# Optimization experiments

Measured on AMD Instinct MI355X. Metric: run time of the kernel, lower is better.

## Reference

```python
import jax, jax.numpy as jnp
import numpy as np
from jax import lax

TAU = 2.0      # tau_s
V_TH = 0.5     # spike threshold
ALPHA = 2.0    # ATan surrogate width

@jax.custom_vjp
def spike_fn(v):
    return (v >= V_TH).astype(v.dtype)

def _spike_fwd(v):
    return spike_fn(v), v

def _spike_bwd(v, g):
    sg = (ALPHA / 2.0) / (1.0 + (jnp.pi / 2.0 * ALPHA * (v - V_TH)) ** 2)
    return (g * sg,)

spike_fn.defvjp(_spike_fwd, _spike_bwd)

T, B, S = 4, 128, 64
D_STATE = D_TAU = D_EVENT = 3136
FUSION, HIDDEN, LAST = 512, 512, 18

def setup_inputs() -> dict:
    key = jax.random.key(0)
    ks = jax.random.split(key, 10)
    def w(k, i, o):
        return jax.random.normal(k, (i, o), jnp.float32) / np.sqrt(i)
    return {
        'state_embedding': jax.random.normal(ks[0], (T, B, D_STATE), jnp.float32),
        'tau_embedding': jax.random.normal(ks[1], (T, B * S, D_TAU), jnp.float32),
        'eventspikes_embedding': jax.random.normal(ks[2], (T, B, D_EVENT), jnp.float32),
        'W_prox': w(ks[3], D_STATE, FUSION),
        'W_dist': w(ks[4], D_TAU, FUSION),
        'W_trunk': w(ks[5], D_EVENT, FUSION),
        'W1': w(ks[6], FUSION, HIDDEN),
        'b1': jnp.zeros((HIDDEN,), jnp.float32),
        'W2': w(ks[7], HIDDEN, LAST),
        'b2': jnp.zeros((LAST,), jnp.float32),
    }

def reference(state_embedding, tau_embedding, eventspikes_embedding,
              W_prox, W_dist, W_trunk, W1, b1, W2, b2):
    t_win, bsz, _ = state_embedding.shape
    ssz = tau_embedding.shape[1] // bsz
    fsz = W_prox.shape[1]
    hsz = W1.shape[1]

    def step(carry, xs):
        p, d, t, soma, lif_mem = carry
        se, te, ee = xs
        prox = (se @ W_prox)[:, None, :]              # [B,1,F]
        dist = (te @ W_dist).reshape(bsz, ssz, fsz)   # [B,S,F]
        trunk = (ee @ W_trunk)[:, None, :]            # [B,1,F]
        # multi-compartment LIF integration
        p = p + (prox - p) / TAU
        d = d + (dist - d) / TAU
        t = t + (trunk - t) / TAU
        soma = soma + (p * d + t - soma) / TAU        # [B,S,F]
        s = spike_fn(soma)
        soma = soma * (1.0 - s)
        emb = s.reshape(bsz * ssz, fsz)
        # _last: Linear -> LIF -> Linear
        h = emb @ W1 + b1
        lif_mem = lif_mem + (h - lif_mem) / TAU
        hs = spike_fn(lif_mem)
        lif_mem = lif_mem * (1.0 - hs)
        out = hs @ W2 + b2                            # [B*S, LAST]
        return (p, d, t, soma, lif_mem), out

    z = jnp.zeros
    init = (z((bsz, 1, fsz)), z((bsz, ssz, fsz)), z((bsz, 1, fsz)),
            z((bsz, ssz, fsz)), z((bsz * ssz, hsz)))
    _, outs = lax.scan(step, init, (state_embedding, tau_embedding, eventspikes_embedding))
    q = outs.mean(0)                                  # average over time window
    return q.reshape(bsz, ssz, -1).transpose(0, 2, 1)  # [B, LAST, S]
```

## Files before the change

### kernel.cpp

```cpp
#include <hip/hip_runtime.h>
#include <stdint.h>

typedef __attribute__((ext_vector_type(4))) float f32x4;

#define T_WIN 4
#define BSZ   128
#define SSZ   64
#define DDIM  3136
#define FDIM  512
#define HDIM  512
#define LDIM  18
#define ROWS  8192
#define KB    16

struct GArgs { const void* A; const float* B; float* C; int M; };

template<int AMODE, int FIRST>
__global__ __launch_bounds__(128, 2) void sgemm_pass(GArgs g0, GArgs g1, GArgs g2,
                                                     int N, int K, int ks, int ke) {
  GArgs g = g0;
  if (blockIdx.z == 1) g = g1;
  else if (blockIdx.z == 2) g = g2;
  const int m0 = blockIdx.x * 128;
  if (m0 >= g.M) return;
  const int n0 = blockIdx.y * 128;

  __shared__ float sA[KB][256];
  __shared__ float sB[KB][132];

  const int tid = threadIdx.x;
  const int tx = tid & 15;
  const int ty = tid >> 4;

  const int am = tid;
  const int br = tid >> 3;
  const int bc = (tid & 7) * 16;

  const float*   Af = (const float*)g.A;
  const uint8_t* A8 = (const uint8_t*)g.A;

  float acc[16][8];
#pragma unroll
  for (int i = 0; i < 16; i++)
#pragma unroll
    for (int j = 0; j < 8; j++) acc[i][j] = 0.f;

  for (int k0 = ks; k0 < ke; k0 += KB) {
    f32x4 av[4];
    if (AMODE == 0) {
      const float* ap = Af + (size_t)(m0 + am) * K + k0;
#pragma unroll
      for (int c = 0; c < 4; c++) av[c] = *(const f32x4*)(ap + 4 * c);
    } else {
      uint4 wrd = *(const uint4*)(A8 + (size_t)(m0 + am) * K + k0);
      uint32_t u[4] = {wrd.x, wrd.y, wrd.z, wrd.w};
#pragma unroll
      for (int c = 0; c < 4; c++) {
        av[c][0] = (float)(u[c] & 255u);
        av[c][1] = (float)((u[c] >> 8) & 255u);
        av[c][2] = (float)((u[c] >> 16) & 255u);
        av[c][3] = (float)((u[c] >> 24) & 255u);
      }
    }
    f32x4 bv[4];
    const float* bp = g.B + (size_t)(k0 + br) * N + n0 + bc;
#pragma unroll
    for (int c = 0; c < 4; c++) bv[c] = *(const f32x4*)(bp + 4 * c);

    __syncthreads();
#pragma unroll
    for (int c = 0; c < 4; c++)
#pragma unroll
      for (int j = 0; j < 4; j++)
        sA[4 * c + j][am] = av[c][j];
#pragma unroll
    for (int c = 0; c < 4; c++)
      *(f32x4*)&sB[br][bc + 4 * c] = bv[c];
    __syncthreads();

#pragma unroll 2
    for (int k = 0; k < KB; k++) {
      f32x4 a0 = *(const f32x4*)&sA[k][ty * 16];
      f32x4 a1 = *(const f32x4*)&sA[k][ty * 16 + 4];
      f32x4 a2 = *(const f32x4*)&sA[k][ty * 16 + 8];
      f32x4 a3 = *(const f32x4*)&sA[k][ty * 16 + 12];
      f32x4 b0 = *(const f32x4*)&sB[k][tx * 4];
      f32x4 b1 = *(const f32x4*)&sB[k][64 + tx * 4];
      float a[16] = {a0[0], a0[1], a0[2], a0[3], a1[0], a1[1], a1[2], a1[3],
                     a2[0], a2[1], a2[2], a2[3], a3[0], a3[1], a3[2], a3[3]};
      float b[8]  = {b0[0], b0[1], b0[2], b0[3], b1[0], b1[1], b1[2], b1[3]};
#pragma unroll
      for (int i = 0; i < 16; i++)
#pragma unroll
        for (int j = 0; j < 8; j++)
          acc[i][j] = __fmaf_rn(a[i], b[j], acc[i][j]);
    }
  }

#pragma unroll
  for (int i = 0; i < 16; i++) {
    float* cp = g.C + (size_t)(m0 + ty * 16 + i) * N + n0;
    f32x4 v0 = {acc[i][0], acc[i][1], acc[i][2], acc[i][3]};
    f32x4 v1 = {acc[i][4], acc[i][5], acc[i][6], acc[i][7]};
    if (FIRST) {
      *(f32x4*)(cp + tx * 4) = v0;
      *(f32x4*)(cp + 64 + tx * 4) = v1;
    } else {
      f32x4 o0 = *(const f32x4*)(cp + tx * 4);
      f32x4 o1 = *(const f32x4*)(cp + 64 + tx * 4);
#pragma unroll
      for (int c = 0; c < 4; c++) { v0[c] = __fadd_rn(o0[c], v0[c]); v1[c] = __fadd_rn(o1[c], v1[c]); }
      *(f32x4*)(cp + tx * 4) = v0;
      *(f32x4*)(cp + 64 + tx * 4) = v1;
    }
  }
}

__global__ __launch_bounds__(256) void filter_pt_kernel(const float* __restrict__ prox,
                                                        const float* __restrict__ trunk,
                                                        float* __restrict__ P,
                                                        float* __restrict__ Tf) {
  int idx = blockIdx.x * 256 + threadIdx.x;
  int b = idx >> 7;
  int fc = (idx & 127) << 2;
  f32x4 p = {0.f, 0.f, 0.f, 0.f}, t = {0.f, 0.f, 0.f, 0.f};
  for (int tt = 0; tt < T_WIN; tt++) {
    size_t o = (size_t)(tt * BSZ + b) * FDIM + fc;
    f32x4 x = *(const f32x4*)&prox[o];
    f32x4 y = *(const f32x4*)&trunk[o];
#pragma unroll
    for (int c = 0; c < 4; c++) {
      p[c] = __fadd_rn(p[c], __fmul_rn(__fsub_rn(x[c], p[c]), 0.5f));
      t[c] = __fadd_rn(t[c], __fmul_rn(__fsub_rn(y[c], t[c]), 0.5f));
    }
    *(f32x4*)&P[o] = p;
    *(f32x4*)&Tf[o] = t;
  }
}

__global__ __launch_bounds__(256) void lif_soma_kernel(const float* __restrict__ dist,
                                                       const float* __restrict__ P,
                                                       const float* __restrict__ Tf,
                                                       uint8_t* __restrict__ emb) {
  int idx = blockIdx.x * 256 + threadIdx.x;
  int r = idx >> 7;
  int fc = (idx & 127) << 2;
  int b = r >> 6;
  f32x4 d = {0.f, 0.f, 0.f, 0.f}, soma = {0.f, 0.f, 0.f, 0.f};
#pragma unroll
  for (int t = 0; t < T_WIN; t++) {
    f32x4 x  = *(const f32x4*)&dist[(size_t)(t * ROWS + r) * FDIM + fc];
    f32x4 pv = *(const f32x4*)&P[(size_t)(t * BSZ + b) * FDIM + fc];
    f32x4 tv = *(const f32x4*)&Tf[(size_t)(t * BSZ + b) * FDIM + fc];
    uint32_t bits = 0;
#pragma unroll
    for (int c = 0; c < 4; c++) {
      d[c] = __fadd_rn(d[c], __fmul_rn(__fsub_rn(x[c], d[c]), 0.5f));
      float pd = __fmul_rn(pv[c], d[c]);
      float u  = __fadd_rn(pd, tv[c]);
      float w  = __fsub_rn(u, soma[c]);
      soma[c] = __fadd_rn(soma[c], __fmul_rn(w, 0.5f));
      if (soma[c] >= 0.5f) { bits |= (1u << (8 * c)); soma[c] = 0.f; }
    }
    *(uint32_t*)&emb[(size_t)(t * ROWS + r) * FDIM + fc] = bits;
  }
}

__global__ __launch_bounds__(256) void lif_hidden_kernel(const float* __restrict__ H,
                                                         const float* __restrict__ b1,
                                                         uint8_t* __restrict__ cnt) {
  int idx = blockIdx.x * 256 + threadIdx.x;
  int r = idx >> 7;
  int fc = (idx & 127) << 2;
  f32x4 bb = *(const f32x4*)&b1[fc];
  f32x4 lif = {0.f, 0.f, 0.f, 0.f};
  uint32_t counts = 0;
#pragma unroll
  for (int t = 0; t < T_WIN; t++) {
    f32x4 h = *(const f32x4*)&H[(size_t)(t * ROWS + r) * FDIM + fc];
#pragma unroll
    for (int c = 0; c < 4; c++) {
      float hv = __fadd_rn(h[c], bb[c]);
      lif[c] = __fadd_rn(lif[c], __fmul_rn(__fsub_rn(hv, lif[c]), 0.5f));
      if (lif[c] >= 0.5f) { counts += (1u << (8 * c)); lif[c] = 0.f; }
    }
  }
  *(uint32_t*)&cnt[(size_t)r * FDIM + fc] = counts;
}

__global__ __launch_bounds__(256) void out_kernel(const uint8_t* __restrict__ cnt,
                                                  const float* __restrict__ W2,
                                                  const float* __restrict__ b2,
                                                  float* __restrict__ out) {
  int idx = blockIdx.x * 256 + threadIdx.x;
  int r = idx / LDIM;
  int j = idx - r * LDIM;
  const uint4* crow = (const uint4*)(cnt + (size_t)r * HDIM);
  float acc = 0.f;
  for (int q = 0; q < HDIM / 16; q++) {
    uint4 wrd = crow[q];
    uint32_t u[4] = {wrd.x, wrd.y, wrd.z, wrd.w};
#pragma unroll
    for (int wq = 0; wq < 4; wq++)
#pragma unroll
      for (int s = 0; s < 4; s++) {
        uint32_t c = (u[wq] >> (8 * s)) & 255u;
        if (c) acc = __fmaf_rn((float)c * 0.25f, W2[(16 * q + 4 * wq + s) * LDIM + j], acc);
      }
  }
  int b = r >> 6, s = r & 63;
  out[(size_t)b * (LDIM * SSZ) + j * SSZ + s] = __fadd_rn(acc, b2[j]);
}


extern "C" void kernel_launch(void* const* d_in, const int* in_sizes, int n_in,
                              void* d_out, int out_size, void* d_ws, size_t ws_size,
                              hipStream_t stream) {
  const float* se     = (const float*)d_in[0];
  const float* te     = (const float*)d_in[1];
  const float* ee     = (const float*)d_in[2];
  const float* Wprox  = (const float*)d_in[3];
  const float* Wdist  = (const float*)d_in[4];
  const float* Wtrunk = (const float*)d_in[5];
  const float* W1     = (const float*)d_in[6];
  const float* b1     = (const float*)d_in[7];
  const float* W2     = (const float*)d_in[8];
  const float* b2     = (const float*)d_in[9];

  char* ws = (char*)d_ws;
  float*   dist_all  = (float*)(ws);
  uint8_t* emb8      = (uint8_t*)(ws + 67108864);
  uint8_t* cnt8      = (uint8_t*)(ws + 83886080);
  float*   prox_raw  = (float*)(ws + 88080384);
  float*   trunk_raw = (float*)(ws + 89128960);
  float*   P         = (float*)(ws + 90177536);
  float*   Tf        = (float*)(ws + 91226112);

  static const int KC[10] = {0, 384, 768, 1152, 1536, 1920, 2304, 2688, 2912, 3136};

  GArgs gd{te, Wdist, dist_all, T_WIN * ROWS};
  GArgs gp{se, Wprox, prox_raw, T_WIN * BSZ};
  GArgs gt{ee, Wtrunk, trunk_raw, T_WIN * BSZ};
  {
    dim3 gg(256, 4, 3), bb(128);
    sgemm_pass<0, 1><<<gg, bb, 0, stream>>>(gd, gp, gt, FDIM, DDIM, KC[0], KC[1]);
    for (int p = 1; p < 9; p++)
      sgemm_pass<0, 0><<<gg, bb, 0, stream>>>(gd, gp, gt, FDIM, DDIM, KC[p], KC[p + 1]);
  }

  filter_pt_kernel<<<64, 256, 0, stream>>>(prox_raw, trunk_raw, P, Tf);

  lif_soma_kernel<<<4096, 256, 0, stream>>>(dist_all, P, Tf, emb8);

  GArgs gh{emb8, W1, dist_all, T_WIN * ROWS};
  {
    dim3 gg(256, 4, 1), bb(128);
    sgemm_pass<1, 1><<<gg, bb, 0, stream>>>(gh, gh, gh, HDIM, FDIM, 0, 256);
    sgemm_pass<1, 0><<<gg, bb, 0, stream>>>(gh, gh, gh, HDIM, FDIM, 256, 512);
  }

  lif_hidden_kernel<<<4096, 256, 0, stream>>>(dist_all, b1, cnt8);

  out_kernel<<<576, 256, 0, stream>>>(cnt8, W2, b2, (float*)d_out);
}
```

Before: 2.403 ms.

## Replace sequential split-K passes with one launch writing per-chunk partials

The nine sequential split-K GEMM launches (each reading back and adding the previous partial) become one launch with the K-chunk on grid z. Each chunk writes its own partial buffer, and the downstream LIF kernels sum the 9 (or 2) partials in the same fixed order. The grid is also compacted so the small prox/trunk GEMMs no longer launch mostly-empty blocks, and the inner loop gains register prefetch of the next tile. This removes per-pass launch gaps and read-modify-write traffic, but the partial buffers take about 600 MB of workspace that the LIF kernels must then read back.

Measured after the change: 2.116 ms. 12.0% less time.

```diff
diff --git a/kernel.cpp b/kernel.cpp
--- a/kernel.cpp
+++ b/kernel.cpp
@@ -15,15 +15,28 @@
 
 struct GArgs { const void* A; const float* B; float* C; int M; };
 
-template<int AMODE, int FIRST>
-__global__ __launch_bounds__(128, 2) void sgemm_pass(GArgs g0, GArgs g1, GArgs g2,
-                                                     int N, int K, int ks, int ke) {
+__device__ __forceinline__ void kchunk3136(int z, int& ks, int& ke) {
+  ks = (z <= 7) ? 384 * z : 2912;
+  ke = (z <= 6) ? 384 * (z + 1) : ((z == 7) ? 2912 : 3136);
+}
+
+template<int AMODE, int SMALLS>
+__global__ __launch_bounds__(128, 2) void gemm_chunks(GArgs g0, GArgs g1, GArgs g2,
+                                                      int N, int K, int kcmode) {
+  int xb = blockIdx.x;
   GArgs g = g0;
-  if (blockIdx.z == 1) g = g1;
-  else if (blockIdx.z == 2) g = g2;
-  const int m0 = blockIdx.x * 128;
-  if (m0 >= g.M) return;
+  if (SMALLS && xb >= 256) {
+    int idx = xb - 256;
+    g = (idx >> 2) ? g2 : g1;
+    xb = idx & 3;
+  }
+  int ks, ke;
+  if (kcmode == 0) kchunk3136(blockIdx.z, ks, ke);
+  else { ks = blockIdx.z * 256; ke = ks + 256; }
+
+  const int m0 = xb * 128;
   const int n0 = blockIdx.y * 128;
+  float* C = g.C + (size_t)blockIdx.z * g.M * N;
 
   __shared__ float sA[KB][256];
   __shared__ float sB[KB][132];
@@ -45,8 +58,8 @@
 #pragma unroll
     for (int j = 0; j < 8; j++) acc[i][j] = 0.f;
 
-  for (int k0 = ks; k0 < ke; k0 += KB) {
-    f32x4 av[4];
+  f32x4 av[4], bv[4];
+  auto load_step = [&](int k0) {
     if (AMODE == 0) {
       const float* ap = Af + (size_t)(m0 + am) * K + k0;
 #pragma unroll
@@ -62,11 +75,13 @@
         av[c][3] = (float)((u[c] >> 24) & 255u);
       }
     }
-    f32x4 bv[4];
     const float* bp = g.B + (size_t)(k0 + br) * N + n0 + bc;
 #pragma unroll
     for (int c = 0; c < 4; c++) bv[c] = *(const f32x4*)(bp + 4 * c);
-
+  };
+
+  load_step(ks);
+  for (int k0 = ks; k0 < ke; k0 += KB) {
     __syncthreads();
 #pragma unroll
     for (int c = 0; c < 4; c++)
@@ -78,7 +93,9 @@
       *(f32x4*)&sB[br][bc + 4 * c] = bv[c];
     __syncthreads();
 
-#pragma unroll 2
+    if (k0 + KB < ke) load_step(k0 + KB);
+
+#pragma unroll 4
     for (int k = 0; k < KB; k++) {
       f32x4 a0 = *(const f32x4*)&sA[k][ty * 16];
       f32x4 a1 = *(const f32x4*)&sA[k][ty * 16 + 4];
@@ -99,35 +116,33 @@
 
 #pragma unroll
   for (int i = 0; i < 16; i++) {
-    float* cp = g.C + (size_t)(m0 + ty * 16 + i) * N + n0;
+    float* cp = C + (size_t)(m0 + ty * 16 + i) * N + n0;
     f32x4 v0 = {acc[i][0], acc[i][1], acc[i][2], acc[i][3]};
     f32x4 v1 = {acc[i][4], acc[i][5], acc[i][6], acc[i][7]};
-    if (FIRST) {
-      *(f32x4*)(cp + tx * 4) = v0;
-      *(f32x4*)(cp + 64 + tx * 4) = v1;
-    } else {
-      f32x4 o0 = *(const f32x4*)(cp + tx * 4);
-      f32x4 o1 = *(const f32x4*)(cp + 64 + tx * 4);
-#pragma unroll
-      for (int c = 0; c < 4; c++) { v0[c] = __fadd_rn(o0[c], v0[c]); v1[c] = __fadd_rn(o1[c], v1[c]); }
-      *(f32x4*)(cp + tx * 4) = v0;
-      *(f32x4*)(cp + 64 + tx * 4) = v1;
-    }
-  }
-}
-
-__global__ __launch_bounds__(256) void filter_pt_kernel(const float* __restrict__ prox,
-                                                        const float* __restrict__ trunk,
-                                                        float* __restrict__ P,
-                                                        float* __restrict__ Tf) {
+    *(f32x4*)(cp + tx * 4) = v0;
+    *(f32x4*)(cp + 64 + tx * 4) = v1;
+  }
+}
+
+__global__ __launch_bounds__(256) void filter_pt9(const float* __restrict__ Cp,
+                                                  const float* __restrict__ Ct,
+                                                  float* __restrict__ P,
+                                                  float* __restrict__ Tf) {
+  const size_t CH = (size_t)T_WIN * BSZ * FDIM;
   int idx = blockIdx.x * 256 + threadIdx.x;
   int b = idx >> 7;
   int fc = (idx & 127) << 2;
   f32x4 p = {0.f, 0.f, 0.f, 0.f}, t = {0.f, 0.f, 0.f, 0.f};
   for (int tt = 0; tt < T_WIN; tt++) {
     size_t o = (size_t)(tt * BSZ + b) * FDIM + fc;
-    f32x4 x = *(const f32x4*)&prox[o];
-    f32x4 y = *(const f32x4*)&trunk[o];
+    f32x4 x = *(const f32x4*)&Cp[o];
+    f32x4 y = *(const f32x4*)&Ct[o];
+    for (int q = 1; q < 9; q++) {
+      f32x4 xq = *(const f32x4*)&Cp[o + q * CH];
+      f32x4 yq = *(const f32x4*)&Ct[o + q * CH];
+#pragma unroll
+      for (int c = 0; c < 4; c++) { x[c] = __fadd_rn(x[c], xq[c]); y[c] = __fadd_rn(y[c], yq[c]); }
+    }
 #pragma unroll
     for (int c = 0; c < 4; c++) {
       p[c] = __fadd_rn(p[c], __fmul_rn(__fsub_rn(x[c], p[c]), 0.5f));
@@ -138,10 +153,11 @@
   }
 }
 
-__global__ __launch_bounds__(256) void lif_soma_kernel(const float* __restrict__ dist,
-                                                       const float* __restrict__ P,
-                                                       const float* __restrict__ Tf,
-                                                       uint8_t* __restrict__ emb) {
+__global__ __launch_bounds__(256) void lif_soma9(const float* __restrict__ Cd,
+                                                 const float* __restrict__ P,
+                                                 const float* __restrict__ Tf,
+                                                 uint8_t* __restrict__ emb) {
+  const size_t CH = (size_t)T_WIN * ROWS * FDIM;
   int idx = blockIdx.x * 256 + threadIdx.x;
   int r = idx >> 7;
   int fc = (idx & 127) << 2;
@@ -149,7 +165,14 @@
   f32x4 d = {0.f, 0.f, 0.f, 0.f}, soma = {0.f, 0.f, 0.f, 0.f};
 #pragma unroll
   for (int t = 0; t < T_WIN; t++) {
-    f32x4 x  = *(const f32x4*)&dist[(size_t)(t * ROWS + r) * FDIM + fc];
+    size_t o = (size_t)(t * ROWS + r) * FDIM + fc;
+    f32x4 x = *(const f32x4*)&Cd[o];
+#pragma unroll
+    for (int q = 1; q < 9; q++) {
+      f32x4 xq = *(const f32x4*)&Cd[o + q * CH];
+#pragma unroll
+      for (int c = 0; c < 4; c++) x[c] = __fadd_rn(x[c], xq[c]);
+    }
     f32x4 pv = *(const f32x4*)&P[(size_t)(t * BSZ + b) * FDIM + fc];
     f32x4 tv = *(const f32x4*)&Tf[(size_t)(t * BSZ + b) * FDIM + fc];
     uint32_t bits = 0;
@@ -162,13 +185,14 @@
       soma[c] = __fadd_rn(soma[c], __fmul_rn(w, 0.5f));
       if (soma[c] >= 0.5f) { bits |= (1u << (8 * c)); soma[c] = 0.f; }
     }
-    *(uint32_t*)&emb[(size_t)(t * ROWS + r) * FDIM + fc] = bits;
-  }
-}
-
-__global__ __launch_bounds__(256) void lif_hidden_kernel(const float* __restrict__ H,
-                                                         const float* __restrict__ b1,
-                                                         uint8_t* __restrict__ cnt) {
+    *(uint32_t*)&emb[o] = bits;
+  }
+}
+
+__global__ __launch_bounds__(256) void lif_hidden2(const float* __restrict__ Hc,
+                                                   const float* __restrict__ b1,
+                                                   uint8_t* __restrict__ cnt) {
+  const size_t CH = (size_t)T_WIN * ROWS * FDIM;
   int idx = blockIdx.x * 256 + threadIdx.x;
   int r = idx >> 7;
   int fc = (idx & 127) << 2;
@@ -177,10 +201,12 @@
   uint32_t counts = 0;
 #pragma unroll
   for (int t = 0; t < T_WIN; t++) {
-    f32x4 h = *(const f32x4*)&H[(size_t)(t * ROWS + r) * FDIM + fc];
+    size_t o = (size_t)(t * ROWS + r) * FDIM + fc;
+    f32x4 h0 = *(const f32x4*)&Hc[o];
+    f32x4 h1 = *(const f32x4*)&Hc[o + CH];
 #pragma unroll
     for (int c = 0; c < 4; c++) {
-      float hv = __fadd_rn(h[c], bb[c]);
+      float hv = __fadd_rn(__fadd_rn(h0[c], h1[c]), bb[c]);
       lif[c] = __fadd_rn(lif[c], __fmul_rn(__fsub_rn(hv, lif[c]), 0.5f));
       if (lif[c] >= 0.5f) { counts += (1u << (8 * c)); lif[c] = 0.f; }
     }
@@ -228,38 +254,28 @@
   const float* b2     = (const float*)d_in[9];
 
   char* ws = (char*)d_ws;
-  float*   dist_all  = (float*)(ws);
-  uint8_t* emb8      = (uint8_t*)(ws + 67108864);
-  uint8_t* cnt8      = (uint8_t*)(ws + 83886080);
-  float*   prox_raw  = (float*)(ws + 88080384);
-  float*   trunk_raw = (float*)(ws + 89128960);
-  float*   P         = (float*)(ws + 90177536);
-  float*   Tf        = (float*)(ws + 91226112);
-
-  static const int KC[10] = {0, 384, 768, 1152, 1536, 1920, 2304, 2688, 2912, 3136};
-
-  GArgs gd{te, Wdist, dist_all, T_WIN * ROWS};
-  GArgs gp{se, Wprox, prox_raw, T_WIN * BSZ};
-  GArgs gt{ee, Wtrunk, trunk_raw, T_WIN * BSZ};
-  {
-    dim3 gg(256, 4, 3), bb(128);
-    sgemm_pass<0, 1><<<gg, bb, 0, stream>>>(gd, gp, gt, FDIM, DDIM, KC[0], KC[1]);
-    for (int p = 1; p < 9; p++)
-      sgemm_pass<0, 0><<<gg, bb, 0, stream>>>(gd, gp, gt, FDIM, DDIM, KC[p], KC[p + 1]);
-  }
-
-  filter_pt_kernel<<<64, 256, 0, stream>>>(prox_raw, trunk_raw, P, Tf);
-
-  lif_soma_kernel<<<4096, 256, 0, stream>>>(dist_all, P, Tf, emb8);
-
-  GArgs gh{emb8, W1, dist_all, T_WIN * ROWS};
-  {
-    dim3 gg(256, 4, 1), bb(128);
-    sgemm_pass<1, 1><<<gg, bb, 0, stream>>>(gh, gh, gh, HDIM, FDIM, 0, 256);
-    sgemm_pass<1, 0><<<gg, bb, 0, stream>>>(gh, gh, gh, HDIM, FDIM, 256, 512);
-  }
-
-  lif_hidden_kernel<<<4096, 256, 0, stream>>>(dist_all, b1, cnt8);
+  float*   Cd   = (float*)(ws);
+  float*   Hc   = (float*)(ws);
+  float*   Cp   = (float*)(ws + 603979776);
+  float*   Ct   = (float*)(ws + 613416960);
+  float*   P    = (float*)(ws + 622854144);
+  float*   Tf   = (float*)(ws + 623902720);
+  uint8_t* emb8 = (uint8_t*)(ws + 624951296);
+  uint8_t* cnt8 = (uint8_t*)(ws + 641728512);
+
+  GArgs gd{te, Wdist, Cd, T_WIN * ROWS};
+  GArgs gp{se, Wprox, Cp, T_WIN * BSZ};
+  GArgs gt{ee, Wtrunk, Ct, T_WIN * BSZ};
+  gemm_chunks<0, 1><<<dim3(264, 4, 9), 128, 0, stream>>>(gd, gp, gt, FDIM, DDIM, 0);
+
+  filter_pt9<<<64, 256, 0, stream>>>(Cp, Ct, P, Tf);
+
+  lif_soma9<<<4096, 256, 0, stream>>>(Cd, P, Tf, emb8);
+
+  GArgs gh{emb8, W1, Hc, T_WIN * ROWS};
+  gemm_chunks<1, 0><<<dim3(256, 4, 2), 128, 0, stream>>>(gh, gh, gh, HDIM, FDIM, 1);
+
+  lif_hidden2<<<4096, 256, 0, stream>>>(Hc, b1, cnt8);
 
   out_kernel<<<576, 256, 0, stream>>>(cnt8, W2, b2, (float*)d_out);
 }
```
